# Performance work log

Measured on AMD Instinct MI355X. Metric: run time of the kernel, lower is better.

## Reference

```python
import jax, jax.numpy as jnp
import numpy as np

B, S, D, F, E, NS, K = 2, 2048, 512, 2048, 8, 2, 2


def setup_inputs() -> dict:
    key = jax.random.key(0)
    ks = jax.random.split(key, 6)
    scale = 0.02

    def p(k, shape):
        return jax.random.normal(k, shape, jnp.float32) * scale

    return {
        "x": jax.random.normal(ks[0], (B, S, D), jnp.float32),
        "gate_w": p(ks[1], (E, D)),
        "gate_b": jnp.zeros((E,), jnp.float32),
        "sw1": p(ks[2], (NS, F, D)),
        "sb1": jnp.zeros((NS, F), jnp.float32),
        "sw2": p(ks[3], (NS, D, F)),
        "sb2": jnp.zeros((NS, D), jnp.float32),
        "rw1": p(ks[4], (E, F, D)),
        "rb1": jnp.zeros((E, F), jnp.float32),
        "rw2": p(ks[5], (E, D, F)),
        "rb2": jnp.zeros((E, D), jnp.float32),
    }


def reference(x, gate_w, gate_b, sw1, sb1, sw2, sb2, rw1, rb1, rw2, rb2):
    b, s, d = x.shape
    t = x.reshape(-1, d)  # [T, D] flatten batch*seq tokens
    T = t.shape[0]

    # ---- shared experts: sum over NS FFNs (GELU exact, matching nn.GELU) ----
    hs = jax.nn.gelu(jnp.einsum('td,nfd->ntf', t, sw1) + sb1[:, None, :],
                     approximate=False)
    shared = jnp.einsum('ntf,ndf->td', hs, sw2) + sb2.sum(axis=0)

    # ---- router: softmax over experts, top-k probs/indices ----
    logits = t @ gate_w.T + gate_b               # [T, E]
    probs = jax.nn.softmax(logits, axis=-1)
    top_v, top_i = jax.lax.top_k(probs, K)       # [T, K]

    # combine weights: cw[t, e] = sum_k top_v[t, k] * (top_i[t, k] == e)
    cw = jnp.zeros_like(probs).at[jnp.arange(T)[:, None], top_i].add(top_v)  # [T, E]

    # ---- routed experts: run each expert FFN over all tokens, combine by cw ----
    # Mathematically identical to the masked gather/scatter loop in the source:
    # tokens with cw[t,e]==0 contribute nothing.
    hr = jax.nn.gelu(jnp.einsum('td,efd->etf', t, rw1) + rb1[:, None, :],
                     approximate=False)          # [E, T, F]
    oe = jnp.einsum('etf,edf->etd', hr, rw2) + rb2[:, None, :]  # [E, T, D]
    routed = jnp.einsum('etd,te->td', oe, cw)    # weighted combine

    return (shared + routed).reshape(b, s, d)
```

## Files before the change

kernel.cpp:

```cpp
#include <hip/hip_runtime.h>
#include <math.h>

typedef unsigned short u16;
typedef __attribute__((ext_vector_type(8))) __bf16 bf16x8;
typedef __attribute__((ext_vector_type(4))) float floatx4;

#define T_TOK 4096
#define DD    512
#define FF    2048
#define EE    8
#define NSH   2

#define BM 128
#define BN 128
#define BK 32
#define LDK 40
#define LDK2 32
#define BT2 64
#define CAP 4096
#define PADF 0x80000000u
#define NSLOT (2 * T_TOK + EE * BM)

__device__ __forceinline__ float bf2f(u16 v) {
  union { unsigned int u; float f; } c; c.u = ((unsigned int)v) << 16; return c.f;
}
__device__ __forceinline__ u16 f2bf(float f) {
  union { float ff; unsigned int u; } c; c.ff = f;
  unsigned int u = c.u;
  u += 0x7fffu + ((u >> 16) & 1u);
  return (u16)(u >> 16);
}
__device__ __forceinline__ float decode(const void* p, size_t idx, int f) {
  return f ? ((const float*)p)[idx] : bf2f(((const u16*)p)[idx]);
}
__device__ __forceinline__ bf16x8 load8(const void* base, size_t idx, int f) {
  if (f) {
    const float* p = (const float*)base + idx;
    float4 a = *(const float4*)p;
    float4 b = *(const float4*)(p + 4);
    union { bf16x8 v; u16 s[8]; } u;
    u.s[0] = f2bf(a.x); u.s[1] = f2bf(a.y); u.s[2] = f2bf(a.z); u.s[3] = f2bf(a.w);
    u.s[4] = f2bf(b.x); u.s[5] = f2bf(b.y); u.s[6] = f2bf(b.z); u.s[7] = f2bf(b.w);
    return u.v;
  }
  return *(const bf16x8*)((const u16*)base + idx);
}

__device__ __forceinline__ void gll16(const void* g, void* l) {
  __builtin_amdgcn_global_load_lds(
      (const __attribute__((address_space(1))) void*)g,
      (__attribute__((address_space(3))) void*)l, 16, 0, 0);
}

__global__ __launch_bounds__(256) void detect_kernel(
    const void* x, const void* gw, const void* sw1, const void* sw2,
    const void* rw1, const void* rw2, int* flags) {
  __shared__ int cnt;
  const void* ptrs[6] = {x, gw, sw1, sw2, rw1, rw2};
  for (int tnum = 0; tnum < 6; ++tnum) {
    if (threadIdx.x == 0) cnt = 0;
    __syncthreads();
    const u16* p = (const u16*)ptrs[tnum];
    int local = 0;
    for (int i = threadIdx.x; i < 4096; i += 256) {
      unsigned ef = (p[i] >> 7) & 0xFFu;
      if (ef >= 0xE0u) ++local;
    }
    if (local) atomicAdd(&cnt, local);
    __syncthreads();
    if (threadIdx.x == 0) flags[tnum] = (cnt >= 16) ? 1 : 0;
    __syncthreads();
  }
  if (threadIdx.x == 0) {
    flags[6] = flags[0];
    flags[7] = 0;
  }
}

__global__ __launch_bounds__(256) void conv_kernel(
    const void* __restrict__ src, u16* __restrict__ dst,
    const int* __restrict__ flags, int idx, size_t n) {
  int f = flags[idx];
  size_t i = ((size_t)blockIdx.x * 256 + threadIdx.x) * 8;
  if (i >= n) return;
  *(bf16x8*)(dst + i) = load8(src, i, f);
}

__global__ __launch_bounds__(256) void router_kernel(
    const void* __restrict__ x, const void* __restrict__ gw,
    const u16* __restrict__ gb, const int* __restrict__ flags,
    float* __restrict__ cw, int2* __restrict__ tix) {
  int wave = threadIdx.x >> 6, lane = threadIdx.x & 63;
  int t = blockIdx.x * 4 + wave;
  int fx = flags[0], fg = flags[1];
  float acc[EE];
#pragma unroll
  for (int e = 0; e < EE; ++e) acc[e] = 0.f;
#pragma unroll
  for (int j = 0; j < DD / 64; ++j) {
    int d = lane + j * 64;
    float xv = decode(x, (size_t)t * DD + d, fx);
#pragma unroll
    for (int e = 0; e < EE; ++e)
      acc[e] += xv * decode(gw, (size_t)e * DD + d, fg);
  }
#pragma unroll
  for (int e = 0; e < EE; ++e) {
    float v = acc[e];
#pragma unroll
    for (int off = 32; off > 0; off >>= 1) v += __shfl_xor(v, off, 64);
    acc[e] = v;
  }
  if (lane == 0) {
    float m = -1e30f;
#pragma unroll
    for (int e = 0; e < EE; ++e) {
      acc[e] += bf2f(gb[e]);
      m = fmaxf(m, acc[e]);
    }
    float p[EE], s = 0.f;
#pragma unroll
    for (int e = 0; e < EE; ++e) { p[e] = expf(acc[e] - m); s += p[e]; }
    int i1 = 0;
#pragma unroll
    for (int e = 1; e < EE; ++e) if (p[e] > p[i1]) i1 = e;
    int i2 = (i1 == 0) ? 1 : 0;
#pragma unroll
    for (int e = 0; e < EE; ++e)
      if (e != i1 && p[e] > p[i2]) i2 = e;
    float inv = 1.0f / s;
#pragma unroll
    for (int e = 0; e < EE; ++e)
      cw[t * EE + e] = (e == i1 || e == i2) ? p[e] * inv : 0.0f;
    tix[t] = make_int2(i1, i2);
  }
}

__global__ void zero_meta(int* meta) {
  if (threadIdx.x < 24) meta[threadIdx.x] = 0;
}
__global__ __launch_bounds__(256) void build_lists(
    const int2* __restrict__ tix, int* __restrict__ meta,
    unsigned* __restrict__ list, int4* __restrict__ srec) {
  int t = blockIdx.x * 256 + threadIdx.x;
  if (t >= T_TOK) return;
  int2 ii = tix[t];
  int p0 = atomicAdd(&meta[ii.x], 1);
  list[(size_t)ii.x * CAP + p0] = (unsigned)t;
  int p1 = atomicAdd(&meta[ii.y], 1);
  list[(size_t)ii.y * CAP + p1] = (unsigned)t;
  srec[t] = make_int4(ii.x, p0, ii.y, p1);
}
__global__ __launch_bounds__(256) void pad_lists(int* meta, unsigned* list) {
  if (threadIdx.x == 0) {
    int off = 0;
    for (int e = 0; e < EE; ++e) {
      int c = meta[e];
      int pc = (c + BM - 1) & ~(BM - 1);
      meta[8 + e] = pc;
      meta[16 + e] = off;
      off += pc;
    }
  }
  __syncthreads();
#pragma unroll
  for (int e = 0; e < EE; ++e) {
    int c = meta[e], pc = meta[8 + e];
    int i = c + threadIdx.x;
    if (i < pc) list[(size_t)e * CAP + i] = PADF;
  }
}

__global__ __launch_bounds__(256) void g1_fused(
    const u16* __restrict__ xb, const u16* __restrict__ s1b,
    const u16* __restrict__ sb1, const u16* __restrict__ r1b,
    const u16* __restrict__ rb1, const unsigned* __restrict__ list,
    const int* __restrict__ meta, u16* __restrict__ Hsh,
    u16* __restrict__ Hrt) {
  int z = blockIdx.z;
  int bm = blockIdx.y * BM;
  int tid = threadIdx.x, lane = tid & 63, wave = tid >> 6;
  int wm = (wave >> 1) * 64, wn = (wave & 1) * 64;
  int r = lane & 15, q = lane >> 4;
  int srow = tid >> 2, sc8 = (tid & 3) * 8;
  const int K = DD;

  __shared__ u16 As[BM * LDK2];
  __shared__ u16 Bs[BN * LDK2];

  const u16 *gA0, *gA1, *gB0;
  int e = 0, ho = 0, bn;
  if (z < 2) {
    bn = (z * 16 + blockIdx.x) * BN;
    gA0 = xb + (size_t)(bm + srow) * K + sc8;
    gA1 = gA0 + (size_t)64 * K;
    gB0 = s1b + (size_t)(bn + srow) * K + sc8;
  } else {
    e = z - 2;
    if (bm >= meta[8 + e]) return;
    ho = meta[16 + e];
    bn = blockIdx.x * BN;
    unsigned t0 = list[(size_t)e * CAP + bm + srow] & 0x7fffffffu;
    unsigned t1 = list[(size_t)e * CAP + bm + srow + 64] & 0x7fffffffu;
    gA0 = xb + (size_t)t0 * K + sc8;
    gA1 = xb + (size_t)t1 * K + sc8;
    gB0 = r1b + (size_t)e * FF * DD + (size_t)(bn + srow) * K + sc8;
  }
  const u16* gB1 = gB0 + (size_t)64 * K;

  floatx4 acc[4][4];
  floatx4 zero = {0.f, 0.f, 0.f, 0.f};
#pragma unroll
  for (int i = 0; i < 4; ++i)
#pragma unroll
    for (int j = 0; j < 4; ++j) acc[i][j] = zero;

  u16* AsW0 = As + wave * 512;
  u16* AsW1 = As + 2048 + wave * 512;
  u16* BsW0 = Bs + wave * 512;
  u16* BsW1 = Bs + 2048 + wave * 512;

  for (int k0 = 0; k0 < K; k0 += BK) {
    __syncthreads();
    gll16(gA0, AsW0); gll16(gA1, AsW1);
    gll16(gB0, BsW0); gll16(gB1, BsW1);
    gA0 += BK; gA1 += BK; gB0 += BK; gB1 += BK;
    __syncthreads();

    bf16x8 af[4], bfr[4];
#pragma unroll
    for (int mi = 0; mi < 4; ++mi)
      af[mi] = *(const bf16x8*)(As + (wm + mi * 16 + r) * LDK2 + q * 8);
#pragma unroll
    for (int ni = 0; ni < 4; ++ni)
      bfr[ni] = *(const bf16x8*)(Bs + (wn + ni * 16 + r) * LDK2 + q * 8);
#pragma unroll
    for (int mi = 0; mi < 4; ++mi)
#pragma unroll
      for (int ni = 0; ni < 4; ++ni)
        acc[mi][ni] = __builtin_amdgcn_mfma_f32_16x16x32_bf16(
            af[mi], bfr[ni], acc[mi][ni], 0, 0, 0);
  }

  if (z < 2) {
#pragma unroll
    for (int mi = 0; mi < 4; ++mi)
#pragma unroll
      for (int ni = 0; ni < 4; ++ni) {
        int col = bn + wn + ni * 16 + r;
        float bv = bf2f(sb1[col]);
#pragma unroll
        for (int rr = 0; rr < 4; ++rr) {
          int row = bm + wm + mi * 16 + q * 4 + rr;
          float v = acc[mi][ni][rr] + bv;
          float g = 0.5f * v * (1.0f + erff(v * 0.70710678118654752f));
          Hsh[(size_t)row * (NSH * FF) + col] = f2bf(g);
        }
      }
  } else {
#pragma unroll
    for (int mi = 0; mi < 4; ++mi)
#pragma unroll
      for (int ni = 0; ni < 4; ++ni) {
        int col = bn + wn + ni * 16 + r;
        float bv = bf2f(rb1[(size_t)e * FF + col]);
#pragma unroll
        for (int rr = 0; rr < 4; ++rr) {
          int slot = bm + wm + mi * 16 + q * 4 + rr;
          float v = acc[mi][ni][rr] + bv;
          float g = 0.5f * v * (1.0f + erff(v * 0.70710678118654752f));
          Hrt[(size_t)(ho + slot) * FF + col] = f2bf(g);
        }
      }
  }
}

__global__ __launch_bounds__(256) void g2_fused(
    const u16* __restrict__ Hsh, const u16* __restrict__ s2b,
    const u16* __restrict__ sb2, const u16* __restrict__ Hrt,
    const u16* __restrict__ r2b, const u16* __restrict__ rb2,
    const unsigned* __restrict__ list, const int* __restrict__ meta,
    const float* __restrict__ cw, float* __restrict__ oacc,
    float* __restrict__ Ort) {
  int z = blockIdx.z;
  int bm = blockIdx.y * BM;
  int bn = blockIdx.x * BN;
  int tid = threadIdx.x, lane = tid & 63, wave = tid >> 6;
  int wm = (wave >> 1) * 64, wn = (wave & 1) * 64;
  int r = lane & 15, q = lane >> 4;
  int srow = tid >> 2, sc8 = (tid & 3) * 8;
  const int K = FF;

  __shared__ u16 As[BM * LDK2];
  __shared__ u16 Bs[BN * LDK2];

  const u16 *gA0, *gA1, *gB0;
  int e = 0, ho = 0;
  if (z < NSH) {
    gA0 = Hsh + (size_t)(bm + srow) * (NSH * FF) + (size_t)z * FF + sc8;
    gA1 = gA0 + (size_t)64 * (NSH * FF);
    gB0 = s2b + (size_t)z * DD * FF + (size_t)(bn + srow) * K + sc8;
  } else {
    e = z - NSH;
    if (bm >= meta[8 + e]) return;
    ho = meta[16 + e];
    gA0 = Hrt + (size_t)(ho + bm + srow) * K + sc8;
    gA1 = gA0 + (size_t)64 * K;
    gB0 = r2b + (size_t)e * DD * FF + (size_t)(bn + srow) * K + sc8;
  }
  const u16* gB1 = gB0 + (size_t)64 * K;

  floatx4 acc[4][4];
  floatx4 zero = {0.f, 0.f, 0.f, 0.f};
#pragma unroll
  for (int i = 0; i < 4; ++i)
#pragma unroll
    for (int j = 0; j < 4; ++j) acc[i][j] = zero;

  u16* AsW0 = As + wave * 512;
  u16* AsW1 = As + 2048 + wave * 512;
  u16* BsW0 = Bs + wave * 512;
  u16* BsW1 = Bs + 2048 + wave * 512;

  for (int k0 = 0; k0 < K; k0 += BK) {
    __syncthreads();
    gll16(gA0, AsW0); gll16(gA1, AsW1);
    gll16(gB0, BsW0); gll16(gB1, BsW1);
    gA0 += BK; gA1 += BK; gB0 += BK; gB1 += BK;
    __syncthreads();

    bf16x8 af[4], bfr[4];
#pragma unroll
    for (int mi = 0; mi < 4; ++mi)
      af[mi] = *(const bf16x8*)(As + (wm + mi * 16 + r) * LDK2 + q * 8);
#pragma unroll
    for (int ni = 0; ni < 4; ++ni)
      bfr[ni] = *(const bf16x8*)(Bs + (wn + ni * 16 + r) * LDK2 + q * 8);
#pragma unroll
    for (int mi = 0; mi < 4; ++mi)
#pragma unroll
      for (int ni = 0; ni < 4; ++ni)
        acc[mi][ni] = __builtin_amdgcn_mfma_f32_16x16x32_bf16(
            af[mi], bfr[ni], acc[mi][ni], 0, 0, 0);
  }

  if (z < NSH) {
    float* op = oacc + (size_t)z * T_TOK * DD;
#pragma unroll
    for (int mi = 0; mi < 4; ++mi)
#pragma unroll
      for (int ni = 0; ni < 4; ++ni) {
        int col = bn + wn + ni * 16 + r;
        float bv = bf2f(sb2[(size_t)z * DD + col]);
#pragma unroll
        for (int rr = 0; rr < 4; ++rr) {
          int row = bm + wm + mi * 16 + q * 4 + rr;
          op[(size_t)row * DD + col] = acc[mi][ni][rr] + bv;
        }
      }
  } else {
#pragma unroll
    for (int mi = 0; mi < 4; ++mi)
#pragma unroll
      for (int rr = 0; rr < 4; ++rr) {
        int slot = bm + wm + mi * 16 + q * 4 + rr;
        unsigned raw = list[(size_t)e * CAP + slot];
        if (raw & PADF) continue;
        float s = cw[raw * EE + e];
#pragma unroll
        for (int ni = 0; ni < 4; ++ni) {
          int col = bn + wn + ni * 16 + r;
          float v = acc[mi][ni][rr] + bf2f(rb2[(size_t)e * DD + col]);
          Ort[(size_t)(ho + slot) * DD + col] = s * v;
        }
      }
  }
}

typedef struct { u16 a, b, c, d; } u16x4;
__global__ __launch_bounds__(256) void combine_out(
    const float* __restrict__ oacc, const float* __restrict__ Ort,
    const int4* __restrict__ srec, const int* __restrict__ meta,
    void* __restrict__ out, const int* __restrict__ flags) {
  int t  = blockIdx.x * 2 + (threadIdx.x >> 7);
  int c4 = (threadIdx.x & 127) * 4;
  int4 sr = srec[t];
  int g0 = meta[16 + sr.x] + sr.y;
  int g1 = meta[16 + sr.z] + sr.w;
  float4 a = *(const float4*)(oacc + (size_t)t * DD + c4);
  float4 b = *(const float4*)(oacc + (size_t)(T_TOK + t) * DD + c4);
  float4 u = *(const float4*)(Ort + (size_t)g0 * DD + c4);
  float4 v = *(const float4*)(Ort + (size_t)g1 * DD + c4);
  float o0 = a.x + b.x + u.x + v.x;
  float o1 = a.y + b.y + u.y + v.y;
  float o2 = a.z + b.z + u.z + v.z;
  float o3 = a.w + b.w + u.w + v.w;
  size_t idx = (size_t)t * DD + c4;
  if (flags[6]) {
    *(float4*)((float*)out + idx) = make_float4(o0, o1, o2, o3);
  } else {
    u16x4 h = {f2bf(o0), f2bf(o1), f2bf(o2), f2bf(o3)};
    *(u16x4*)((u16*)out + idx) = h;
  }
}

__device__ __forceinline__ void gemm_core(const void* A, size_t aoff, int fA,
                                          const void* B, size_t boff, int fB,
                                          int K, u16* As, u16* Bs,
                                          floatx4 acc[4][4]) {
  int tid  = threadIdx.x;
  int lane = tid & 63, wave = tid >> 6;
  int wm = (wave >> 1) * 64, wn = (wave & 1) * 64;
  int r = lane & 15, q = lane >> 4;
  int srow = tid >> 2;
  int sc8  = (tid & 3) * 8;
  size_t abase = aoff + (size_t)srow * K + sc8;
  size_t bbase = boff + (size_t)srow * K + sc8;
  const size_t half = (size_t)64 * K;

  for (int k0 = 0; k0 < K; k0 += BK) {
    bf16x8 av0 = load8(A, abase + k0, fA);
    bf16x8 av1 = load8(A, abase + half + k0, fA);
    bf16x8 bv0 = load8(B, bbase + k0, fB);
    bf16x8 bv1 = load8(B, bbase + half + k0, fB);
    __syncthreads();
    *(bf16x8*)(As + srow * LDK + sc8)        = av0;
    *(bf16x8*)(As + (srow + 64) * LDK + sc8) = av1;
    *(bf16x8*)(Bs + srow * LDK + sc8)        = bv0;
    *(bf16x8*)(Bs + (srow + 64) * LDK + sc8) = bv1;
    __syncthreads();

    bf16x8 af[4], bfr[4];
#pragma unroll
    for (int mi = 0; mi < 4; ++mi)
      af[mi] = *(const bf16x8*)(As + (wm + mi * 16 + r) * LDK + q * 8);
#pragma unroll
    for (int ni = 0; ni < 4; ++ni)
      bfr[ni] = *(const bf16x8*)(Bs + (wn + ni * 16 + r) * LDK + q * 8);
#pragma unroll
    for (int mi = 0; mi < 4; ++mi)
#pragma unroll
      for (int ni = 0; ni < 4; ++ni)
        acc[mi][ni] = __builtin_amdgcn_mfma_f32_16x16x32_bf16(
            af[mi], bfr[ni], acc[mi][ni], 0, 0, 0);
  }
}

__global__ __launch_bounds__(256) void gemm1_gelu(
    const void* __restrict__ A, size_t aoff, const void* __restrict__ B,
    size_t boff, const u16* __restrict__ bias, size_t bioff,
    u16* __restrict__ H, const int* __restrict__ flags, int iA, int iB,
    int N, int K) {
  __shared__ u16 As[BM * LDK];
  __shared__ u16 Bs[BN * LDK];
  int fA = flags[iA], fB = flags[iB];
  floatx4 acc[4][4];
  floatx4 zero = {0.f, 0.f, 0.f, 0.f};
#pragma unroll
  for (int i = 0; i < 4; ++i)
#pragma unroll
    for (int j = 0; j < 4; ++j) acc[i][j] = zero;

  int bm = blockIdx.y * BM, bn = blockIdx.x * BN;
  gemm_core(A, aoff + (size_t)bm * K, fA, B, boff + (size_t)bn * K, fB, K,
            As, Bs, acc);

  int tid = threadIdx.x, wave = tid >> 6, lane = tid & 63;
  int wm = (wave >> 1) * 64, wn = (wave & 1) * 64;
  int r = lane & 15, q = lane >> 4;
#pragma unroll
  for (int mi = 0; mi < 4; ++mi)
#pragma unroll
    for (int ni = 0; ni < 4; ++ni) {
      int col = bn + wn + ni * 16 + r;
      float bv = bf2f(bias[bioff + col]);
#pragma unroll
      for (int rr = 0; rr < 4; ++rr) {
        int row = bm + wm + mi * 16 + q * 4 + rr;
        float v = acc[mi][ni][rr] + bv;
        float g = 0.5f * v * (1.0f + erff(v * 0.70710678118654752f));
        H[(size_t)row * N + col] = f2bf(g);
      }
    }
}

__global__ __launch_bounds__(256) void gemm2_acc(
    const u16* __restrict__ A, const void* __restrict__ B, size_t boff,
    const u16* __restrict__ bias, size_t bioff, float* __restrict__ outf,
    void* __restrict__ outb, const float* __restrict__ cw,
    const int* __restrict__ flags, int iB, int expert, int accum,
    int row0, int N, int K) {
  __shared__ u16 As[BT2 * LDK];
  __shared__ u16 Bs[BT2 * LDK];
  int fB = flags[iB], fO = flags[6];
  floatx4 acc[2][2];
  floatx4 zero = {0.f, 0.f, 0.f, 0.f};
#pragma unroll
  for (int i = 0; i < 2; ++i)
#pragma unroll
    for (int j = 0; j < 2; ++j) acc[i][j] = zero;

  int bm = blockIdx.y * BT2, bn = blockIdx.x * BT2;
  int tid  = threadIdx.x;
  int lane = tid & 63, wave = tid >> 6;
  int wm = (wave >> 1) * 32, wn = (wave & 1) * 32;
  int r = lane & 15, q = lane >> 4;
  int srow = tid >> 2;
  int sc8  = (tid & 3) * 8;
  size_t abase = (size_t)(bm + srow) * K + sc8;
  size_t bbase = boff + (size_t)(bn + srow) * K + sc8;

  for (int k0 = 0; k0 < K; k0 += BK) {
    bf16x8 av = *(const bf16x8*)(A + abase + k0);
    bf16x8 bv = load8(B, bbase + k0, fB);
    __syncthreads();
    *(bf16x8*)(As + srow * LDK + sc8) = av;
    *(bf16x8*)(Bs + srow * LDK + sc8) = bv;
    __syncthreads();

    bf16x8 af[2], bfr[2];
#pragma unroll
    for (int mi = 0; mi < 2; ++mi)
      af[mi] = *(const bf16x8*)(As + (wm + mi * 16 + r) * LDK + q * 8);
#pragma unroll
    for (int ni = 0; ni < 2; ++ni)
      bfr[ni] = *(const bf16x8*)(Bs + (wn + ni * 16 + r) * LDK + q * 8);
#pragma unroll
    for (int mi = 0; mi < 2; ++mi)
#pragma unroll
      for (int ni = 0; ni < 2; ++ni)
        acc[mi][ni] = __builtin_amdgcn_mfma_f32_16x16x32_bf16(
            af[mi], bfr[ni], acc[mi][ni], 0, 0, 0);
  }

#pragma unroll
  for (int mi = 0; mi < 2; ++mi)
#pragma unroll
    for (int rr = 0; rr < 4; ++rr) {
      int grow = row0 + bm + wm + mi * 16 + q * 4 + rr;
      float s = cw ? cw[grow * EE + expert] : 1.0f;
#pragma unroll
      for (int ni = 0; ni < 2; ++ni) {
        int col = bn + wn + ni * 16 + r;
        float v = acc[mi][ni][rr] + bf2f(bias[bioff + col]);
        size_t idx = (size_t)grow * N + col;
        if (outf) {
          float prev = accum ? outf[idx] : 0.0f;
          outf[idx] = prev + s * v;
        } else if (fO) {
          float* ob = (float*)outb;
          float prev = accum ? ob[idx] : 0.0f;
          ob[idx] = prev + s * v;
        } else {
          u16* ob = (u16*)outb;
          float prev = accum ? bf2f(ob[idx]) : 0.0f;
          ob[idx] = f2bf(prev + s * v);
        }
      }
    }
}

__global__ __launch_bounds__(256) void convert_out(
    const float* __restrict__ acc, void* __restrict__ out,
    const int* __restrict__ flags, int n) {
  int i = blockIdx.x * blockDim.x + threadIdx.x;
  if (i >= n) return;
  if (flags[6]) ((float*)out)[i] = acc[i];
  else ((u16*)out)[i] = f2bf(acc[i]);
}

extern "C" void kernel_launch(void* const* d_in, const int* in_sizes, int n_in,
                              void* d_out, int out_size, void* d_ws, size_t ws_size,
                              hipStream_t stream) {
  (void)in_sizes; (void)n_in; (void)out_size;
  const void* x   = d_in[0];
  const void* gw  = d_in[1];
  const u16*  gb  = (const u16*)d_in[2];
  const void* sw1 = d_in[3];
  const u16*  sb1 = (const u16*)d_in[4];
  const void* sw2 = d_in[5];
  const u16*  sb2 = (const u16*)d_in[6];
  const void* rw1 = d_in[7];
  const u16*  rb1 = (const u16*)d_in[8];
  const void* rw2 = d_in[9];
  const u16*  rb2 = (const u16*)d_in[10];

  const size_t NX   = (size_t)T_TOK * DD;
  const size_t NW1S = (size_t)NSH * FF * DD;
  const size_t NW1R = (size_t)EE * FF * DD;
  const size_t NW2S = (size_t)NSH * DD * FF;
  const size_t NW2R = (size_t)EE * DD * FF;

  size_t off = 0;
  const size_t flO   = off; off += 256;
  const size_t cwO   = off; off += (size_t)T_TOK * EE * 4;
  const size_t tixO  = off; off += (size_t)T_TOK * 8;
  const size_t metaO = off; off += 256;
  const size_t listO = off; off += (size_t)EE * CAP * 4;
  const size_t srecO = off; off += (size_t)T_TOK * 16;
  const size_t accO  = off; off += (size_t)NSH * T_TOK * DD * 4;
  const size_t hshO  = off; off += (size_t)T_TOK * NSH * FF * 2;
  const size_t hrtO  = off; off += (size_t)NSLOT * FF * 2;
  const size_t ortO  = off; off += (size_t)NSLOT * DD * 4;
  const size_t xbO   = off; off += NX * 2;
  const size_t s1O   = off; off += NW1S * 2;
  const size_t r1O   = off; off += NW1R * 2;
  const size_t s2O   = off; off += NW2S * 2;
  const size_t r2O   = off; off += NW2R * 2;
  const int fast = (off <= ws_size) ? 1 : 0;

  char* ws = (char*)d_ws;
  int*   flags = (int*)(ws + flO);
  float* cw    = (float*)(ws + cwO);
  dim3 blk(256);

  detect_kernel<<<1, 256, 0, stream>>>(x, gw, sw1, sw2, rw1, rw2, flags);

  if (fast) {
    int2*     tix  = (int2*)(ws + tixO);
    int*      meta = (int*)(ws + metaO);
    unsigned* list = (unsigned*)(ws + listO);
    int4*     srec = (int4*)(ws + srecO);
    float*    oacc = (float*)(ws + accO);
    u16*      Hsh  = (u16*)(ws + hshO);
    u16*      Hrt  = (u16*)(ws + hrtO);
    float*    Ort  = (float*)(ws + ortO);
    u16*      xb   = (u16*)(ws + xbO);
    u16*      s1b  = (u16*)(ws + s1O);
    u16*      r1b  = (u16*)(ws + r1O);
    u16*      s2b  = (u16*)(ws + s2O);
    u16*      r2b  = (u16*)(ws + r2O);

    conv_kernel<<<NX   / 2048, 256, 0, stream>>>(x,   xb,  flags, 0, NX);
    conv_kernel<<<NW1S / 2048, 256, 0, stream>>>(sw1, s1b, flags, 2, NW1S);
    conv_kernel<<<NW1R / 2048, 256, 0, stream>>>(rw1, r1b, flags, 4, NW1R);
    conv_kernel<<<NW2S / 2048, 256, 0, stream>>>(sw2, s2b, flags, 3, NW2S);
    conv_kernel<<<NW2R / 2048, 256, 0, stream>>>(rw2, r2b, flags, 5, NW2R);
    router_kernel<<<T_TOK / 4, 256, 0, stream>>>(x, gw, gb, flags, cw, tix);
    zero_meta<<<1, 64, 0, stream>>>(meta);
    build_lists<<<T_TOK / 256, 256, 0, stream>>>(tix, meta, list, srec);
    pad_lists<<<1, 256, 0, stream>>>(meta, list);

    dim3 gf1(16, T_TOK / BM, 2 + EE);
    g1_fused<<<gf1, blk, 0, stream>>>(xb, s1b, sb1, r1b, rb1, list, meta,
                                      Hsh, Hrt);
    dim3 gf2(DD / BN, CAP / BM, NSH + EE);
    g2_fused<<<gf2, blk, 0, stream>>>(Hsh, s2b, sb2, Hrt, r2b, rb2, list,
                                      meta, cw, oacc, Ort);
    combine_out<<<T_TOK / 2, 256, 0, stream>>>(oacc, Ort, srec, meta, d_out,
                                               flags);
    return;
  }

  const size_t flB = 256, cwB = (size_t)T_TOK * EE * 4, tixB = (size_t)T_TOK * 8;
  const size_t accB = (size_t)T_TOK * DD * 4;
  static const int tcs[4] = {4096, 2048, 1024, 512};
  int TC = 0, use_f32 = 1;
  for (int i = 0; i < 4; ++i)
    if (flB + cwB + tixB + accB + (size_t)tcs[i] * FF * 2 <= ws_size) { TC = tcs[i]; break; }
  if (!TC) {
    use_f32 = 0;
    for (int i = 0; i < 4; ++i)
      if (flB + cwB + tixB + (size_t)tcs[i] * FF * 2 <= ws_size) { TC = tcs[i]; break; }
  }
  if (!TC) { TC = 512; use_f32 = 0; }

  int2*  tix     = (int2*)(ws + flB + cwB);
  float* out_acc = use_f32 ? (float*)(ws + flB + cwB + tixB) : nullptr;
  u16*   H       = (u16*)(ws + flB + cwB + tixB + (use_f32 ? accB : 0));

  router_kernel<<<T_TOK / 4, 256, 0, stream>>>(x, gw, gb, flags, cw, tix);
  dim3 g1(FF / BN, TC / BM);
  dim3 g2(DD / BT2, TC / BT2);
  const int nchunk = T_TOK / TC;
  for (int f = 0; f < NSH + EE; ++f) {
    const void *w1, *w2; const u16 *b1, *b2; const float* cwp;
    int expert, i1, i2v; size_t w1off, w2off, b1off, b2off;
    if (f < NSH) {
      w1 = sw1; w2 = sw2; b1 = sb1; b2 = sb2;
      w1off = (size_t)f * FF * DD; w2off = (size_t)f * DD * FF;
      b1off = (size_t)f * FF; b2off = (size_t)f * DD;
      cwp = nullptr; expert = 0; i1 = 2; i2v = 3;
    } else {
      int e = f - NSH;
      w1 = rw1; w2 = rw2; b1 = rb1; b2 = rb2;
      w1off = (size_t)e * FF * DD; w2off = (size_t)e * DD * FF;
      b1off = (size_t)e * FF; b2off = (size_t)e * DD;
      cwp = cw; expert = e; i1 = 4; i2v = 5;
    }
    int accum = (f > 0) ? 1 : 0;
    for (int c = 0; c < nchunk; ++c) {
      size_t t0 = (size_t)c * TC;
      gemm1_gelu<<<g1, blk, 0, stream>>>(x, t0 * DD, w1, w1off, b1, b1off, H,
                                         flags, 0, i1, FF, DD);
      gemm2_acc<<<g2, blk, 0, stream>>>(H, w2, w2off, b2, b2off, out_acc,
                                        d_out, cwp, flags, i2v, expert, accum,
                                        (int)t0, DD, FF);
    }
  }
  if (use_f32)
    convert_out<<<(T_TOK * DD) / 256, 256, 0, stream>>>(out_acc, d_out, flags,
                                                        T_TOK * DD);
}
```

Measured before the change: 363.7 us.

## Double-buffer GEMM LDS tiles, fuse setup kernels, and use polynomial GELU

The two grouped GEMM kernels get double-buffered LDS tiles, so the next K-slice loads while MFMAs run on the current one, with one barrier per iteration instead of two. The five conversion launches become one conv_all kernel. Zeroing meta moves into detect_kernel and list building into the router kernel, which cuts launches. Exact erff GELU is replaced by an Abramowitz-Stegun erf approximation with a fast reciprocal and exp, a small accuracy cost and double the LDS per block.

New measurement: 436.9 us. 20.1% more time.

```diff
diff --git a/kernel.cpp b/kernel.cpp
--- a/kernel.cpp
+++ b/kernel.cpp
@@ -46,15 +46,38 @@
   return *(const bf16x8*)((const u16*)base + idx);
 }
 
+__device__ __forceinline__ float fast_gelu(float v) {
+  float x  = v * 0.70710678118654752f;
+  float ax = fabsf(x);
+  float t  = __builtin_amdgcn_rcpf(fmaf(0.3275911f, ax, 1.0f));
+  float p  = fmaf(t, 1.061405429f, -1.453152027f);
+  p = fmaf(t, p, 1.421413741f);
+  p = fmaf(t, p, -0.284496736f);
+  p = fmaf(t, p, 0.254829592f);
+  p = p * t;
+  float e  = __expf(-ax * ax);
+  float er = fmaf(-p, e, 1.0f);
+  er = (x < 0.f) ? -er : er;
+  return 0.5f * v * (1.0f + er);
+}
+
 __device__ __forceinline__ void gll16(const void* g, void* l) {
   __builtin_amdgcn_global_load_lds(
       (const __attribute__((address_space(1))) void*)g,
       (__attribute__((address_space(3))) void*)l, 16, 0, 0);
 }
+__device__ __forceinline__ void stage4(const u16* gA0, const u16* gA1,
+                                       const u16* gB0, const u16* gB1,
+                                       u16* Asb, u16* Bsb, int wave, int k0) {
+  gll16(gA0 + k0, Asb + wave * 512);
+  gll16(gA1 + k0, Asb + 2048 + wave * 512);
+  gll16(gB0 + k0, Bsb + wave * 512);
+  gll16(gB1 + k0, Bsb + 2048 + wave * 512);
+}
 
 __global__ __launch_bounds__(256) void detect_kernel(
     const void* x, const void* gw, const void* sw1, const void* sw2,
-    const void* rw1, const void* rw2, int* flags) {
+    const void* rw1, const void* rw2, int* flags, int* meta) {
   __shared__ int cnt;
   const void* ptrs[6] = {x, gw, sw1, sw2, rw1, rw2};
   for (int tnum = 0; tnum < 6; ++tnum) {
@@ -75,21 +98,41 @@
     flags[6] = flags[0];
     flags[7] = 0;
   }
-}
-
-__global__ __launch_bounds__(256) void conv_kernel(
-    const void* __restrict__ src, u16* __restrict__ dst,
-    const int* __restrict__ flags, int idx, size_t n) {
-  int f = flags[idx];
-  size_t i = ((size_t)blockIdx.x * 256 + threadIdx.x) * 8;
-  if (i >= n) return;
-  *(bf16x8*)(dst + i) = load8(src, i, f);
+  if (meta && threadIdx.x < 24) meta[threadIdx.x] = 0;
+}
+
+#define U8_X  (T_TOK * DD / 8)
+#define U8_S1 (NSH * FF * DD / 8)
+#define U8_R1 (EE * FF * DD / 8)
+#define U8_S2 (NSH * DD * FF / 8)
+#define U8_R2 (EE * DD * FF / 8)
+#define U8_C0 (U8_X)
+#define U8_C1 (U8_C0 + U8_S1)
+#define U8_C2 (U8_C1 + U8_R1)
+#define U8_C3 (U8_C2 + U8_S2)
+#define U8_C4 (U8_C3 + U8_R2)
+__global__ __launch_bounds__(256) void conv_all(
+    const void* __restrict__ x, const void* __restrict__ sw1,
+    const void* __restrict__ rw1, const void* __restrict__ sw2,
+    const void* __restrict__ rw2, u16* __restrict__ xb,
+    u16* __restrict__ s1b, u16* __restrict__ r1b, u16* __restrict__ s2b,
+    u16* __restrict__ r2b, const int* __restrict__ flags) {
+  size_t u = (size_t)blockIdx.x * 256 + threadIdx.x;
+  const void* src; u16* dst; int fi; size_t base;
+  if (u < U8_C0)      { src = x;   dst = xb;  fi = 0; base = 0; }
+  else if (u < U8_C1) { src = sw1; dst = s1b; fi = 2; base = U8_C0; }
+  else if (u < U8_C2) { src = rw1; dst = r1b; fi = 4; base = U8_C1; }
+  else if (u < U8_C3) { src = sw2; dst = s2b; fi = 3; base = U8_C2; }
+  else                { src = rw2; dst = r2b; fi = 5; base = U8_C3; }
+  size_t i = (u - base) * 8;
+  *(bf16x8*)(dst + i) = load8(src, i, flags[fi]);
 }
 
 __global__ __launch_bounds__(256) void router_kernel(
     const void* __restrict__ x, const void* __restrict__ gw,
     const u16* __restrict__ gb, const int* __restrict__ flags,
-    float* __restrict__ cw, int2* __restrict__ tix) {
+    float* __restrict__ cw, int2* __restrict__ tix, int* __restrict__ meta,
+    unsigned* __restrict__ list, int4* __restrict__ srec) {
   int wave = threadIdx.x >> 6, lane = threadIdx.x & 63;
   int t = blockIdx.x * 4 + wave;
   int fx = flags[0], fg = flags[1];
@@ -133,24 +176,16 @@
     for (int e = 0; e < EE; ++e)
       cw[t * EE + e] = (e == i1 || e == i2) ? p[e] * inv : 0.0f;
     tix[t] = make_int2(i1, i2);
-  }
-}
-
-__global__ void zero_meta(int* meta) {
-  if (threadIdx.x < 24) meta[threadIdx.x] = 0;
-}
-__global__ __launch_bounds__(256) void build_lists(
-    const int2* __restrict__ tix, int* __restrict__ meta,
-    unsigned* __restrict__ list, int4* __restrict__ srec) {
-  int t = blockIdx.x * 256 + threadIdx.x;
-  if (t >= T_TOK) return;
-  int2 ii = tix[t];
-  int p0 = atomicAdd(&meta[ii.x], 1);
-  list[(size_t)ii.x * CAP + p0] = (unsigned)t;
-  int p1 = atomicAdd(&meta[ii.y], 1);
-  list[(size_t)ii.y * CAP + p1] = (unsigned)t;
-  srec[t] = make_int4(ii.x, p0, ii.y, p1);
-}
+    if (srec) {
+      int p0 = atomicAdd(&meta[i1], 1);
+      list[(size_t)i1 * CAP + p0] = (unsigned)t;
+      int p1 = atomicAdd(&meta[i2], 1);
+      list[(size_t)i2 * CAP + p1] = (unsigned)t;
+      srec[t] = make_int4(i1, p0, i2, p1);
+    }
+  }
+}
+
 __global__ __launch_bounds__(256) void pad_lists(int* meta, unsigned* list) {
   if (threadIdx.x == 0) {
     int off = 0;
@@ -170,6 +205,7 @@
     if (i < pc) list[(size_t)e * CAP + i] = PADF;
   }
 }
+
 
 __global__ __launch_bounds__(256) void g1_fused(
     const u16* __restrict__ xb, const u16* __restrict__ s1b,
@@ -185,8 +221,8 @@
   int srow = tid >> 2, sc8 = (tid & 3) * 8;
   const int K = DD;
 
-  __shared__ u16 As[BM * LDK2];
-  __shared__ u16 Bs[BN * LDK2];
+  __shared__ u16 As[2][BM * LDK2];
+  __shared__ u16 Bs[2][BN * LDK2];
 
   const u16 *gA0, *gA1, *gB0;
   int e = 0, ho = 0, bn;
@@ -215,31 +251,27 @@
 #pragma unroll
     for (int j = 0; j < 4; ++j) acc[i][j] = zero;
 
-  u16* AsW0 = As + wave * 512;
-  u16* AsW1 = As + 2048 + wave * 512;
-  u16* BsW0 = Bs + wave * 512;
-  u16* BsW1 = Bs + 2048 + wave * 512;
-
+  stage4(gA0, gA1, gB0, gB1, As[0], Bs[0], wave, 0);
+  __syncthreads();
+  int cur = 0;
   for (int k0 = 0; k0 < K; k0 += BK) {
-    __syncthreads();
-    gll16(gA0, AsW0); gll16(gA1, AsW1);
-    gll16(gB0, BsW0); gll16(gB1, BsW1);
-    gA0 += BK; gA1 += BK; gB0 += BK; gB1 += BK;
-    __syncthreads();
-
+    if (k0 + BK < K)
+      stage4(gA0, gA1, gB0, gB1, As[cur ^ 1], Bs[cur ^ 1], wave, k0 + BK);
     bf16x8 af[4], bfr[4];
 #pragma unroll
     for (int mi = 0; mi < 4; ++mi)
-      af[mi] = *(const bf16x8*)(As + (wm + mi * 16 + r) * LDK2 + q * 8);
+      af[mi] = *(const bf16x8*)(As[cur] + (wm + mi * 16 + r) * LDK2 + q * 8);
 #pragma unroll
     for (int ni = 0; ni < 4; ++ni)
-      bfr[ni] = *(const bf16x8*)(Bs + (wn + ni * 16 + r) * LDK2 + q * 8);
+      bfr[ni] = *(const bf16x8*)(Bs[cur] + (wn + ni * 16 + r) * LDK2 + q * 8);
 #pragma unroll
     for (int mi = 0; mi < 4; ++mi)
 #pragma unroll
       for (int ni = 0; ni < 4; ++ni)
         acc[mi][ni] = __builtin_amdgcn_mfma_f32_16x16x32_bf16(
             af[mi], bfr[ni], acc[mi][ni], 0, 0, 0);
+    __syncthreads();
+    cur ^= 1;
   }
 
   if (z < 2) {
@@ -253,8 +285,7 @@
         for (int rr = 0; rr < 4; ++rr) {
           int row = bm + wm + mi * 16 + q * 4 + rr;
           float v = acc[mi][ni][rr] + bv;
-          float g = 0.5f * v * (1.0f + erff(v * 0.70710678118654752f));
-          Hsh[(size_t)row * (NSH * FF) + col] = f2bf(g);
+          Hsh[(size_t)row * (NSH * FF) + col] = f2bf(fast_gelu(v));
         }
       }
   } else {
@@ -268,8 +299,7 @@
         for (int rr = 0; rr < 4; ++rr) {
           int slot = bm + wm + mi * 16 + q * 4 + rr;
           float v = acc[mi][ni][rr] + bv;
-          float g = 0.5f * v * (1.0f + erff(v * 0.70710678118654752f));
-          Hrt[(size_t)(ho + slot) * FF + col] = f2bf(g);
+          Hrt[(size_t)(ho + slot) * FF + col] = f2bf(fast_gelu(v));
         }
       }
   }
@@ -291,8 +321,8 @@
   int srow = tid >> 2, sc8 = (tid & 3) * 8;
   const int K = FF;
 
-  __shared__ u16 As[BM * LDK2];
-  __shared__ u16 Bs[BN * LDK2];
+  __shared__ u16 As[2][BM * LDK2];
+  __shared__ u16 Bs[2][BN * LDK2];
 
   const u16 *gA0, *gA1, *gB0;
   int e = 0, ho = 0;
@@ -317,31 +347,27 @@
 #pragma unroll
     for (int j = 0; j < 4; ++j) acc[i][j] = zero;
 
-  u16* AsW0 = As + wave * 512;
-  u16* AsW1 = As + 2048 + wave * 512;
-  u16* BsW0 = Bs + wave * 512;
-  u16* BsW1 = Bs + 2048 + wave * 512;
-
+  stage4(gA0, gA1, gB0, gB1, As[0], Bs[0], wave, 0);
+  __syncthreads();
+  int cur = 0;
   for (int k0 = 0; k0 < K; k0 += BK) {
-    __syncthreads();
-    gll16(gA0, AsW0); gll16(gA1, AsW1);
-    gll16(gB0, BsW0); gll16(gB1, BsW1);
-    gA0 += BK; gA1 += BK; gB0 += BK; gB1 += BK;
-    __syncthreads();
-
+    if (k0 + BK < K)
+      stage4(gA0, gA1, gB0, gB1, As[cur ^ 1], Bs[cur ^ 1], wave, k0 + BK);
     bf16x8 af[4], bfr[4];
 #pragma unroll
     for (int mi = 0; mi < 4; ++mi)
-      af[mi] = *(const bf16x8*)(As + (wm + mi * 16 + r) * LDK2 + q * 8);
+      af[mi] = *(const bf16x8*)(As[cur] + (wm + mi * 16 + r) * LDK2 + q * 8);
 #pragma unroll
     for (int ni = 0; ni < 4; ++ni)
-      bfr[ni] = *(const bf16x8*)(Bs + (wn + ni * 16 + r) * LDK2 + q * 8);
+      bfr[ni] = *(const bf16x8*)(Bs[cur] + (wn + ni * 16 + r) * LDK2 + q * 8);
 #pragma unroll
     for (int mi = 0; mi < 4; ++mi)
 #pragma unroll
       for (int ni = 0; ni < 4; ++ni)
         acc[mi][ni] = __builtin_amdgcn_mfma_f32_16x16x32_bf16(
             af[mi], bfr[ni], acc[mi][ni], 0, 0, 0);
+    __syncthreads();
+    cur ^= 1;
   }
 
   if (z < NSH) {
@@ -478,8 +504,7 @@
       for (int rr = 0; rr < 4; ++rr) {
         int row = bm + wm + mi * 16 + q * 4 + rr;
         float v = acc[mi][ni][rr] + bv;
-        float g = 0.5f * v * (1.0f + erff(v * 0.70710678118654752f));
-        H[(size_t)row * N + col] = f2bf(g);
+        H[(size_t)row * N + col] = f2bf(fast_gelu(v));
       }
     }
 }
@@ -614,8 +639,6 @@
   float* cw    = (float*)(ws + cwO);
   dim3 blk(256);
 
-  detect_kernel<<<1, 256, 0, stream>>>(x, gw, sw1, sw2, rw1, rw2, flags);
-
   if (fast) {
     int2*     tix  = (int2*)(ws + tixO);
     int*      meta = (int*)(ws + metaO);
@@ -631,14 +654,12 @@
     u16*      s2b  = (u16*)(ws + s2O);
     u16*      r2b  = (u16*)(ws + r2O);
 
-    conv_kernel<<<NX   / 2048, 256, 0, stream>>>(x,   xb,  flags, 0, NX);
-    conv_kernel<<<NW1S / 2048, 256, 0, stream>>>(sw1, s1b, flags, 2, NW1S);
-    conv_kernel<<<NW1R / 2048, 256, 0, stream>>>(rw1, r1b, flags, 4, NW1R);
-    conv_kernel<<<NW2S / 2048, 256, 0, stream>>>(sw2, s2b, flags, 3, NW2S);
-    conv_kernel<<<NW2R / 2048, 256, 0, stream>>>(rw2, r2b, flags, 5, NW2R);
-    router_kernel<<<T_TOK / 4, 256, 0, stream>>>(x, gw, gb, flags, cw, tix);
-    zero_meta<<<1, 64, 0, stream>>>(meta);
-    build_lists<<<T_TOK / 256, 256, 0, stream>>>(tix, meta, list, srec);
+    detect_kernel<<<1, 256, 0, stream>>>(x, gw, sw1, sw2, rw1, rw2, flags,
+                                         meta);
+    conv_all<<<U8_C4 / 256, 256, 0, stream>>>(x, sw1, rw1, sw2, rw2, xb, s1b,
+                                              r1b, s2b, r2b, flags);
+    router_kernel<<<T_TOK / 4, 256, 0, stream>>>(x, gw, gb, flags, cw, tix,
+                                                 meta, list, srec);
     pad_lists<<<1, 256, 0, stream>>>(meta, list);
 
     dim3 gf1(16, T_TOK / BM, 2 + EE);
@@ -652,6 +673,8 @@
     return;
   }
 
+  detect_kernel<<<1, 256, 0, stream>>>(x, gw, sw1, sw2, rw1, rw2, flags,
+                                       nullptr);
   const size_t flB = 256, cwB = (size_t)T_TOK * EE * 4, tixB = (size_t)T_TOK * 8;
   const size_t accB = (size_t)T_TOK * DD * 4;
   static const int tcs[4] = {4096, 2048, 1024, 512};
@@ -669,7 +692,8 @@
   float* out_acc = use_f32 ? (float*)(ws + flB + cwB + tixB) : nullptr;
   u16*   H       = (u16*)(ws + flB + cwB + tixB + (use_f32 ? accB : 0));
 
-  router_kernel<<<T_TOK / 4, 256, 0, stream>>>(x, gw, gb, flags, cw, tix);
+  router_kernel<<<T_TOK / 4, 256, 0, stream>>>(x, gw, gb, flags, cw, tix,
+                                               nullptr, nullptr, nullptr);
   dim3 g1(FF / BN, TC / BM);
   dim3 g2(DD / BT2, TC / BT2);
   const int nchunk = T_TOK / TC;
```
